# Kernel optimization log

Measured on AMD Instinct MI355X. Metric: run time of the kernel, lower is better.

The kernel has to match this reference:

```python
import jax, jax.numpy as jnp
import numpy as np

B, C, H, W, R = 4, 64, 64, 64, 16  # batch, channels, height, width, reduced_channels
EPS = 1e-5


def setup_inputs() -> dict:
    key = jax.random.key(0)
    ks = jax.random.split(key, 10)
    s = 1.0 / np.sqrt(C)
    sf = 1.0 / np.sqrt(R)
    return {
        "x": jax.random.normal(ks[0], (B, C, H, W), jnp.float32),
        "y": jax.random.normal(ks[1], (B, C, H, W), jnp.float32),
        "Wq": jax.random.normal(ks[2], (R, C), jnp.float32) * s,
        "bq": jax.random.normal(ks[3], (R,), jnp.float32) * s,
        "Wk": jax.random.normal(ks[4], (R, C), jnp.float32) * s,
        "bk": jax.random.normal(ks[5], (R,), jnp.float32) * s,
        "Wv": jax.random.normal(ks[6], (R, C), jnp.float32) * s,
        "bv": jax.random.normal(ks[7], (R,), jnp.float32) * s,
        "Wf": jax.random.normal(ks[8], (C, R), jnp.float32) * sf,
        "bf": jax.random.normal(ks[9], (C,), jnp.float32) * sf,
        "ln_w": jnp.ones((C, H, W), jnp.float32),   # fresh nn.LayerNorm -> weight=1
        "ln_b": jnp.zeros((C, H, W), jnp.float32),  # fresh nn.LayerNorm -> bias=0
        "channels": C,
        "shape": H,
    }


def reference(x, y, Wq, bq, Wk, bk, Wv, bv, Wf, bf, ln_w, ln_b, channels, shape):
    b, c, h, w = x.shape
    xf = x.reshape(b, c, h * w)  # [B, C, N]
    yf = y.reshape(b, c, h * w)
    # 1x1 convs == per-pixel matmuls
    q = jnp.einsum('rc,bcn->brn', Wq, xf) + bq[None, :, None]   # [B, R, N]
    k = jnp.einsum('rc,bcn->brn', Wk, yf) + bk[None, :, None]
    v = jnp.einsum('rc,bcn->brn', Wv, yf) + bv[None, :, None]
    # unscaled attention: softmax(q^T k) over key axis
    attn = jax.nn.softmax(jnp.einsum('brn,brm->bnm', q, k), axis=-1)  # [B, N, N]
    out = jnp.einsum('brm,bnm->brn', v, attn)                          # [B, R, N]
    out = jnp.einsum('cr,brn->bcn', Wf, out) + bf[None, :, None]       # final 1x1 conv
    out = out.reshape(b, c, h, w) + x                                  # residual
    # LayerNorm over (C, H, W)
    mean = out.mean(axis=(1, 2, 3), keepdims=True)
    var = out.var(axis=(1, 2, 3), keepdims=True)
    out = (out - mean) * jax.lax.rsqrt(var + EPS) * ln_w + ln_b
    return out
```

## Files before the change

### kernel.cpp

```cpp
#include <hip/hip_runtime.h>
#include <hip/hip_bf16.h>
#include <math.h>

namespace {
constexpr int Bn = 4;
constexpr int Cn = 64;
constexpr int Nn = 4096;
constexpr int Rn = 16;
constexpr int Sn = 16;
constexpr int KPS = Nn / Sn;
constexpr int Tn = Nn / 16;
}

typedef __attribute__((ext_vector_type(4))) short v4s;
typedef __attribute__((ext_vector_type(4))) float v4f;

__device__ inline unsigned short f2bf(float f) {
    union { float f; unsigned u; } v; v.f = f;
    unsigned r = v.u + 0x7fffu + ((v.u >> 16) & 1u);
    return (unsigned short)(r >> 16);
}

__device__ inline unsigned pkbf(float a, float b) {
    __hip_bfloat162 t = __float22bfloat162_rn(make_float2(a, b));
    union { __hip_bfloat162 h; unsigned u; } v; v.h = t;
    return v.u;
}

__global__ __launch_bounds__(256) void qkv_proj(
    const float* __restrict__ x, const float* __restrict__ y,
    const float* __restrict__ Wq, const float* __restrict__ bq,
    const float* __restrict__ Wk, const float* __restrict__ bk,
    const float* __restrict__ Wv, const float* __restrict__ bv,
    unsigned short* __restrict__ q2, unsigned short* __restrict__ k2,
    unsigned short* __restrict__ v2)
{
    const int job = blockIdx.x >> 8;
    const int rem = blockIdx.x & 255;
    const int b = rem >> 6;
    const int n = ((rem & 63) << 6) + (threadIdx.x & 63);
    const int rq = threadIdx.x >> 6;

    const float* src  = (job == 0) ? x : y;
    const float* W    = (job == 0) ? Wq : (job == 1 ? Wk : Wv);
    const float* bias = (job == 0) ? bq : (job == 1 ? bk : bv);

    const float* sp = src + (size_t)b * Cn * Nn + n;
    const float* wp = W + rq * 4 * Cn;

    float o0 = bias[rq*4+0], o1 = bias[rq*4+1], o2 = bias[rq*4+2], o3 = bias[rq*4+3];
#pragma unroll
    for (int c = 0; c < Cn; ++c) {
        const float xc = sp[(size_t)c * Nn];
        o0 += wp[c] * xc;
        o1 += wp[Cn + c] * xc;
        o2 += wp[2*Cn + c] * xc;
        o3 += wp[3*Cn + c] * xc;
    }

    if (job == 2) {
        unsigned short* vp = v2 + ((size_t)b * Rn + rq*4) * Nn + n;
        vp[0]              = f2bf(o0);
        vp[(size_t)Nn]     = f2bf(o1);
        vp[(size_t)2*Nn]   = f2bf(o2);
        vp[(size_t)3*Nn]   = f2bf(o3);
    } else {
        unsigned short* dst = (job == 0 ? q2 : k2) + ((size_t)(b*Nn + n)) * Rn + rq*4;
        unsigned long long pk = (unsigned long long)pkbf(o0, o1)
                              | ((unsigned long long)pkbf(o2, o3) << 32);
        *(unsigned long long*)dst = pk;
    }
}

__global__ __launch_bounds__(256) void attn_mfma(
    const unsigned short* __restrict__ q2, const unsigned short* __restrict__ k2,
    const unsigned short* __restrict__ v2,
    float* __restrict__ Pl, float* __restrict__ Pacc)
{
    const int lane = threadIdx.x & 63;
    const int wid  = threadIdx.x >> 6;
    const int bid  = blockIdx.x;
    const int b   = bid >> 8;
    const int rem = bid & 255;
    const int s   = rem >> 4;
    const int tbase = ((rem & 15) * 4 + wid) * 4;

    const int col = lane & 15;
    const int g4  = (lane >> 4) << 2;

    v4s qf[4];
#pragma unroll
    for (int i = 0; i < 4; ++i)
        qf[i] = *(const v4s*)(q2 + ((size_t)(b*Nn + (tbase+i)*16 + col)) * Rn + g4);

    const unsigned short* kp = k2 + ((size_t)(b*Nn + s*KPS) + col) * Rn + g4;
    const unsigned short* vp = v2 + ((size_t)b*Rn + col) * Nn + s*KPS + g4;

    const v4f zf = {0.f, 0.f, 0.f, 0.f};
    v4f oacc[4] = {zf, zf, zf, zf};
    float l[4] = {0.f, 0.f, 0.f, 0.f};

#pragma unroll 4
    for (int kt = 0; kt < KPS/16; ++kt) {
        const v4s kf = *(const v4s*)(kp + kt * 16 * Rn);
        const v4s vf = *(const v4s*)(vp + kt * 16);

#pragma unroll
        for (int i = 0; i < 4; ++i) {
            v4f st = __builtin_amdgcn_mfma_f32_16x16x16bf16_1k(kf, qf[i], zf, 0, 0, 0);
            const float p0 = __expf(st[0]), p1 = __expf(st[1]);
            const float p2 = __expf(st[2]), p3 = __expf(st[3]);
            l[i] += (p0 + p1) + (p2 + p3);
            union { unsigned u[2]; v4s v; } uu;
            uu.u[0] = pkbf(p0, p1); uu.u[1] = pkbf(p2, p3);
            oacc[i] = __builtin_amdgcn_mfma_f32_16x16x16bf16_1k(vf, uu.v, oacc[i], 0, 0, 0);
        }
    }

#pragma unroll
    for (int i = 0; i < 4; ++i) {
        l[i] += __shfl_xor(l[i], 16);
        l[i] += __shfl_xor(l[i], 32);
    }
    if (lane < 16) {
#pragma unroll
        for (int i = 0; i < 4; ++i)
            Pl[(size_t)(b*Sn + s) * Nn + (tbase+i)*16 + lane] = l[i];
    }

#pragma unroll
    for (int i = 0; i < 4; ++i) {
        float4 a = make_float4(oacc[i][0], oacc[i][1], oacc[i][2], oacc[i][3]);
        *(float4*)(Pacc + ((size_t)((b*Tn + tbase+i)*Sn + s) * 64 + lane) * 4) = a;
    }
}

__global__ __launch_bounds__(256) void epilogue_fused(
    const float* __restrict__ Pacc, const float* __restrict__ Pl,
    const float* __restrict__ Wf, const float* __restrict__ bfb,
    const float* __restrict__ x,
    float* __restrict__ zout, float* __restrict__ sums)
{
    const int lane = threadIdx.x & 63;
    const int wid  = threadIdx.x >> 6;
    const int wv   = blockIdx.x * 4 + wid;
    const int b = wv >> 8;
    const int t = wv & 255;
    const int col = lane & 15;

    float4 acc = make_float4(0.f, 0.f, 0.f, 0.f);
#pragma unroll
    for (int s = 0; s < Sn; ++s) {
        const float4 p = *(const float4*)(Pacc + ((size_t)((b*Tn + t)*Sn + s) * 64 + lane) * 4);
        acc.x += p.x; acc.y += p.y; acc.z += p.z; acc.w += p.w;
    }

    float L = 0.f;
#pragma unroll
    for (int s = 0; s < Sn; ++s)
        L += Pl[(size_t)(b*Sn + s) * Nn + t*16 + col];
    const float invL = 1.f / L;

    float os[4] = {acc.x * invL, acc.y * invL, acc.z * invL, acc.w * invL};

    float orv[Rn];
#pragma unroll
    for (int k = 0; k < 4; ++k)
#pragma unroll
        for (int j = 0; j < 4; ++j)
            orv[k*4+j] = __shfl(os[j], col + 16*k);

    const int cg = lane >> 4;
    const int n = t*16 + col;
    const float* xp = x + (size_t)b * Cn * Nn + n;
    float* zp = zout + (size_t)b * Cn * Nn + n;

    float s1 = 0.f, s2 = 0.f;
#pragma unroll
    for (int cc = 0; cc < 16; ++cc) {
        const int c = cg * 16 + cc;
        const float4 w0 = *(const float4*)(Wf + c*Rn);
        const float4 w1 = *(const float4*)(Wf + c*Rn + 4);
        const float4 w2 = *(const float4*)(Wf + c*Rn + 8);
        const float4 w3 = *(const float4*)(Wf + c*Rn + 12);
        float z = bfb[c] + xp[(size_t)c * Nn];
        z += w0.x*orv[0]  + w0.y*orv[1]  + w0.z*orv[2]  + w0.w*orv[3];
        z += w1.x*orv[4]  + w1.y*orv[5]  + w1.z*orv[6]  + w1.w*orv[7];
        z += w2.x*orv[8]  + w2.y*orv[9]  + w2.z*orv[10] + w2.w*orv[11];
        z += w3.x*orv[12] + w3.y*orv[13] + w3.z*orv[14] + w3.w*orv[15];
        zp[(size_t)c * Nn] = z;
        s1 += z;
        s2 += z * z;
    }

#pragma unroll
    for (int off = 32; off > 0; off >>= 1) {
        s1 += __shfl_down(s1, off);
        s2 += __shfl_down(s2, off);
    }
    __shared__ float red[8];
    if ((threadIdx.x & 63) == 0) { red[wid] = s1; red[4 + wid] = s2; }
    __syncthreads();
    if (threadIdx.x == 0) {
        atomicAdd(&sums[2 * b + 0], red[0] + red[1] + red[2] + red[3]);
        atomicAdd(&sums[2 * b + 1], red[4] + red[5] + red[6] + red[7]);
    }
}

__global__ __launch_bounds__(256) void ln_apply(
    float* __restrict__ out, const float* __restrict__ lnw,
    const float* __restrict__ lnb, const float* __restrict__ sums)
{
    const int i = blockIdx.x * blockDim.x + threadIdx.x;
    const int b = i >> 16;
    const int jw = i & 65535;

    const float invM = 1.0f / (float)(Cn * Nn);
    const float S1 = sums[2 * b + 0];
    const float S2 = sums[2 * b + 1];
    const float mean = S1 * invM;
    const float var = fmaxf(S2 * invM - mean * mean, 0.0f);
    const float rs = rsqrtf(var + 1e-5f);

    float4 z = ((const float4*)out)[i];
    const float4 w = ((const float4*)lnw)[jw];
    const float4 bb = ((const float4*)lnb)[jw];
    z.x = (z.x - mean) * rs * w.x + bb.x;
    z.y = (z.y - mean) * rs * w.y + bb.y;
    z.z = (z.z - mean) * rs * w.z + bb.z;
    z.w = (z.w - mean) * rs * w.w + bb.w;
    ((float4*)out)[i] = z;
}

extern "C" void kernel_launch(void* const* d_in, const int* in_sizes, int n_in,
                              void* d_out, int out_size, void* d_ws, size_t ws_size,
                              hipStream_t stream) {
    const float* x   = (const float*)d_in[0];
    const float* y   = (const float*)d_in[1];
    const float* Wq  = (const float*)d_in[2];
    const float* bq  = (const float*)d_in[3];
    const float* Wk  = (const float*)d_in[4];
    const float* bk  = (const float*)d_in[5];
    const float* Wv  = (const float*)d_in[6];
    const float* bv  = (const float*)d_in[7];
    const float* Wf  = (const float*)d_in[8];
    const float* bfv = (const float*)d_in[9];
    const float* lnw = (const float*)d_in[10];
    const float* lnb = (const float*)d_in[11];
    float* out = (float*)d_out;

    char* p = (char*)d_ws;
    unsigned short* q2 = (unsigned short*)p; p += (size_t)Bn*Nn*Rn*2;
    unsigned short* k2 = (unsigned short*)p; p += (size_t)Bn*Nn*Rn*2;
    unsigned short* v2 = (unsigned short*)p; p += (size_t)Bn*Nn*Rn*2;
    float* Pl   = (float*)p; p += (size_t)Bn*Sn*Nn*4;
    float* Pacc = (float*)p; p += (size_t)Bn*Tn*Sn*64*4*4;
    float* sums = (float*)p;

    hipMemsetAsync(sums, 0, 2 * Bn * sizeof(float), stream);
    qkv_proj<<<768, 256, 0, stream>>>(x, y, Wq, bq, Wk, bk, Wv, bv, q2, k2, v2);
    attn_mfma<<<Bn * Sn * (Tn/4) / 4, 256, 0, stream>>>(q2, k2, v2, Pl, Pacc);
    epilogue_fused<<<Bn * Tn / 4, 256, 0, stream>>>(Pacc, Pl, Wf, bfv, x, out, sums);
    ln_apply<<<(Bn * Cn * Nn / 4) / 256, 256, 0, stream>>>(out, lnw, lnb, sums);
}
```

Measured before the change: 136.7 us.

## Fuse K/V projection, pre-tile V for MFMA, fold memset into projection kernel

The K and V projections now share one pass over y, so y is read once for both instead of twice, and the grid shrinks from 768 to 512 blocks. V is written in a layout pre-tiled to the MFMA fragment order, so each lane in the attention kernel does one contiguous 8-byte load per key tile instead of strided row reads. The memset of the LayerNorm sum buffer is replaced by a write from block 0 of the projection kernel, removing one launch. The attention key loop is also fully unrolled; the cost is scattered 2-byte V stores and more register pressure in both kernels.

```diff
diff --git a/kernel.cpp b/kernel.cpp
--- a/kernel.cpp
+++ b/kernel.cpp
@@ -33,48 +33,66 @@
     const float* __restrict__ Wk, const float* __restrict__ bk,
     const float* __restrict__ Wv, const float* __restrict__ bv,
     unsigned short* __restrict__ q2, unsigned short* __restrict__ k2,
-    unsigned short* __restrict__ v2)
-{
+    unsigned short* __restrict__ v3, float* __restrict__ sums)
+{
+    if (blockIdx.x == 0 && threadIdx.x < 2 * Bn) sums[threadIdx.x] = 0.0f;
+
     const int job = blockIdx.x >> 8;
     const int rem = blockIdx.x & 255;
     const int b = rem >> 6;
     const int n = ((rem & 63) << 6) + (threadIdx.x & 63);
     const int rq = threadIdx.x >> 6;
 
-    const float* src  = (job == 0) ? x : y;
-    const float* W    = (job == 0) ? Wq : (job == 1 ? Wk : Wv);
-    const float* bias = (job == 0) ? bq : (job == 1 ? bk : bv);
-
-    const float* sp = src + (size_t)b * Cn * Nn + n;
-    const float* wp = W + rq * 4 * Cn;
-
-    float o0 = bias[rq*4+0], o1 = bias[rq*4+1], o2 = bias[rq*4+2], o3 = bias[rq*4+3];
-#pragma unroll
-    for (int c = 0; c < Cn; ++c) {
-        const float xc = sp[(size_t)c * Nn];
-        o0 += wp[c] * xc;
-        o1 += wp[Cn + c] * xc;
-        o2 += wp[2*Cn + c] * xc;
-        o3 += wp[3*Cn + c] * xc;
-    }
-
-    if (job == 2) {
-        unsigned short* vp = v2 + ((size_t)b * Rn + rq*4) * Nn + n;
-        vp[0]              = f2bf(o0);
-        vp[(size_t)Nn]     = f2bf(o1);
-        vp[(size_t)2*Nn]   = f2bf(o2);
-        vp[(size_t)3*Nn]   = f2bf(o3);
-    } else {
-        unsigned short* dst = (job == 0 ? q2 : k2) + ((size_t)(b*Nn + n)) * Rn + rq*4;
+    const float* sp = (job == 0 ? x : y) + (size_t)b * Cn * Nn + n;
+
+    if (job == 0) {
+        const float* wp = Wq + rq * 4 * Cn;
+        float o0 = bq[rq*4+0], o1 = bq[rq*4+1], o2 = bq[rq*4+2], o3 = bq[rq*4+3];
+#pragma unroll
+        for (int c = 0; c < Cn; ++c) {
+            const float xc = sp[(size_t)c * Nn];
+            o0 += wp[c] * xc;
+            o1 += wp[Cn + c] * xc;
+            o2 += wp[2*Cn + c] * xc;
+            o3 += wp[3*Cn + c] * xc;
+        }
+        unsigned short* dst = q2 + ((size_t)(b*Nn + n)) * Rn + rq*4;
         unsigned long long pk = (unsigned long long)pkbf(o0, o1)
                               | ((unsigned long long)pkbf(o2, o3) << 32);
         *(unsigned long long*)dst = pk;
+    } else {
+        const float* wk = Wk + rq * 4 * Cn;
+        const float* wv = Wv + rq * 4 * Cn;
+        float k0 = bk[rq*4+0], k1 = bk[rq*4+1], k2v = bk[rq*4+2], k3 = bk[rq*4+3];
+        float u0 = bv[rq*4+0], u1 = bv[rq*4+1], u2 = bv[rq*4+2], u3 = bv[rq*4+3];
+#pragma unroll
+        for (int c = 0; c < Cn; ++c) {
+            const float xc = sp[(size_t)c * Nn];
+            k0 += wk[c] * xc;        k1 += wk[Cn + c] * xc;
+            k2v += wk[2*Cn + c] * xc; k3 += wk[3*Cn + c] * xc;
+            u0 += wv[c] * xc;        u1 += wv[Cn + c] * xc;
+            u2 += wv[2*Cn + c] * xc; u3 += wv[3*Cn + c] * xc;
+        }
+        unsigned short* dk = k2 + ((size_t)(b*Nn + n)) * Rn + rq*4;
+        unsigned long long pk = (unsigned long long)pkbf(k0, k1)
+                              | ((unsigned long long)pkbf(k2v, k3) << 32);
+        *(unsigned long long*)dk = pk;
+
+        const int s  = n >> 8;
+        const int kt = (n >> 4) & 15;
+        const int ko = n & 15;
+        unsigned short* vt = v3 + (((size_t)(b*Sn + s)*16 + kt) << 8)
+                                + ((ko >> 2) << 6) + (ko & 3);
+        vt[(rq*4+0)*4] = f2bf(u0);
+        vt[(rq*4+1)*4] = f2bf(u1);
+        vt[(rq*4+2)*4] = f2bf(u2);
+        vt[(rq*4+3)*4] = f2bf(u3);
     }
 }
 
 __global__ __launch_bounds__(256) void attn_mfma(
     const unsigned short* __restrict__ q2, const unsigned short* __restrict__ k2,
-    const unsigned short* __restrict__ v2,
+    const unsigned short* __restrict__ v3,
     float* __restrict__ Pl, float* __restrict__ Pacc)
 {
     const int lane = threadIdx.x & 63;
@@ -94,16 +112,16 @@
         qf[i] = *(const v4s*)(q2 + ((size_t)(b*Nn + (tbase+i)*16 + col)) * Rn + g4);
 
     const unsigned short* kp = k2 + ((size_t)(b*Nn + s*KPS) + col) * Rn + g4;
-    const unsigned short* vp = v2 + ((size_t)b*Rn + col) * Nn + s*KPS + g4;
+    const unsigned short* vtile = v3 + (((size_t)(b*Sn + s)) << 12);
 
     const v4f zf = {0.f, 0.f, 0.f, 0.f};
     v4f oacc[4] = {zf, zf, zf, zf};
     float l[4] = {0.f, 0.f, 0.f, 0.f};
 
-#pragma unroll 4
+#pragma unroll
     for (int kt = 0; kt < KPS/16; ++kt) {
         const v4s kf = *(const v4s*)(kp + kt * 16 * Rn);
-        const v4s vf = *(const v4s*)(vp + kt * 16);
+        const v4s vf = *(const v4s*)(vtile + (kt << 8) + (lane << 2));
 
 #pragma unroll
         for (int i = 0; i < 4; ++i) {
@@ -252,14 +270,13 @@
     char* p = (char*)d_ws;
     unsigned short* q2 = (unsigned short*)p; p += (size_t)Bn*Nn*Rn*2;
     unsigned short* k2 = (unsigned short*)p; p += (size_t)Bn*Nn*Rn*2;
-    unsigned short* v2 = (unsigned short*)p; p += (size_t)Bn*Nn*Rn*2;
+    unsigned short* v3 = (unsigned short*)p; p += (size_t)Bn*Nn*Rn*2;
     float* Pl   = (float*)p; p += (size_t)Bn*Sn*Nn*4;
     float* Pacc = (float*)p; p += (size_t)Bn*Tn*Sn*64*4*4;
     float* sums = (float*)p;
 
-    hipMemsetAsync(sums, 0, 2 * Bn * sizeof(float), stream);
-    qkv_proj<<<768, 256, 0, stream>>>(x, y, Wq, bq, Wk, bk, Wv, bv, q2, k2, v2);
-    attn_mfma<<<Bn * Sn * (Tn/4) / 4, 256, 0, stream>>>(q2, k2, v2, Pl, Pacc);
+    qkv_proj<<<512, 256, 0, stream>>>(x, y, Wq, bq, Wk, bk, Wv, bv, q2, k2, v3, sums);
+    attn_mfma<<<Bn * Sn * (Tn/4) / 4, 256, 0, stream>>>(q2, k2, v3, Pl, Pacc);
     epilogue_fused<<<Bn * Tn / 4, 256, 0, stream>>>(Pacc, Pl, Wf, bfv, x, out, sums);
     ln_apply<<<(Bn * Cn * Nn / 4) / 256, 256, 0, stream>>>(out, lnw, lnb, sums);
 }
```

New measurement: 135.6 us. No clear change (-0.8%).
